# Performance work log

Hardware: AMD Instinct MI355X
Metric: run time of the kernel (lower is better)

## Reference

```python
import jax, jax.numpy as jnp
from jax import lax
import numpy as np
import math

# ---- static hyperparameters (from init_kwargs) ----
NUM_RAY = 64
NUM_RAY2 = NUM_RAY * NUM_RAY
NUM_SAMPLE = 64
STEP = 1.0 / (NUM_SAMPLE - 1)
RK = 3                       # RK4Range: neighbor cube side
K = 64                       # Num_RIGuassKernel per axis
PH = (192, 192, 192)         # PhantomSize (D, H, W)
THETA_X, THETA_Y, THETA_Z = 0.1, 0.05, 0.02
CENTER = (0.5, 0.5, 0.5)

# ---- constant neighbor offsets and kernel-center grids (Process_Parameter) ----
half = (RK - 1) // 2
_r = np.arange(-half, half + 1)
Xr_np, Yr_np, Zr_np = np.meshgrid(_r, _r, _r)
XR = jnp.asarray(Xr_np.flatten().reshape(1, RK ** 3), dtype=jnp.float32)
YR = jnp.asarray(Yr_np.flatten().reshape(1, RK ** 3), dtype=jnp.float32)
ZR = jnp.asarray(Zr_np.flatten().reshape(1, RK ** 3), dtype=jnp.float32)
_c = np.linspace(0, 1, K, dtype='float32')
Xc_np, Yc_np, Zc_np = np.meshgrid(_c, _c, _c)
XC = jnp.asarray(Xc_np.flatten())
YC = jnp.asarray(Yc_np.flatten())
ZC = jnp.asarray(Zc_np.flatten())

# ---- rotation matrices (Theta2TransMatrix) ----
def _build_transmats():
    def ry(t):
        c, s = math.cos(t), math.sin(t)
        return np.array([[1, 0, 0, 0], [0, c, -s, 0], [0, s, c, 0], [0, 0, 0, 1]], dtype=np.float64)
    def rx(t):
        c, s = math.cos(t), math.sin(t)
        return np.array([[c, 0, -s, 0], [0, 1, 0, 0], [s, 0, c, 0], [0, 0, 0, 1]], dtype=np.float64)
    def rz(t):
        c, s = math.cos(t), math.sin(t)
        return np.array([[c, -s, 0, 0], [s, c, 0, 0], [0, 0, 1, 0], [0, 0, 0, 1]], dtype=np.float64)
    RY, RY_ = ry(-THETA_Y), ry(THETA_Y)
    RX, RX_ = rx(THETA_X), rx(-THETA_X)
    RZ, RZ_ = rz(-THETA_Z), rz(THETA_Z)
    cx, cy, cz = CENTER
    S1 = np.eye(4); S1[3, :3] = [-cx, -cy, -cz]
    S2 = np.eye(4); S2[3, :3] = [cx, cy, cz]
    M_crd = S1 @ RZ @ RY @ RX @ S2
    M_drv = RX_ @ RY_ @ RZ_
    return jnp.asarray(M_crd, dtype=jnp.float32), jnp.asarray(M_drv, dtype=jnp.float32)

M_CRD, M_DRV = _build_transmats()


def _indexdist(x, y, z, RI):
    # x,y,z: [N]; RI: [K^3, 2] -> Gaussian-kernel interpolated n and spatial derivatives
    X, Y, Z = x[:, None], y[:, None], z[:, None]
    Xn = jnp.clip(jnp.round(X * K) + XR, 0.0, K - 1.0)
    Yn = jnp.clip(jnp.round(Y * K) + YR, 0.0, K - 1.0)
    Zn = jnp.clip(jnp.round(Z * K) + ZR, 0.0, K - 1.0)
    lin = (K * K * Yn + K * Xn + Zn).astype(jnp.int32)   # [N, RK^3]
    dx = XC[lin] - X
    dy = YC[lin] - Y
    dz = ZC[lin] - Z
    A = RI[lin, 0]
    sig = RI[lin, 1]
    inv_s2 = 1.0 / (sig * sig)
    ni = jnp.exp(-(dx * dx + dy * dy + dz * dz) * 0.5 * inv_s2) + 2e-7
    norm = jnp.sum(ni, axis=1)
    nu = ni * A
    nx = jnp.sum(nu * dx * inv_s2, axis=1)
    ny = jnp.sum(nu * dy * inv_s2, axis=1)
    nz = jnp.sum(nu * dz * inv_s2, axis=1)
    ndx = jnp.sum(ni * dx * inv_s2, axis=1)
    ndy = jnp.sum(ni * dy * inv_s2, axis=1)
    ndz = jnp.sum(ni * dz * inv_s2, axis=1)
    nu_s = jnp.sum(nu, axis=1)
    n = nu_s / norm
    inv_norm2 = 1.0 / (norm * norm)
    nx = (norm * nx - nu_s * ndx) * inv_norm2
    ny = (norm * ny - nu_s * ndy) * inv_norm2
    nz = (norm * nz - nu_s * ndz) * inv_norm2
    return n, nx, ny, nz


def _rayeq(z0, xy0, RI):
    ones = jnp.ones_like(z0)
    t = jnp.stack([xy0[:, 2], xy0[:, 0], z0, ones], axis=1) @ M_CRD
    n, dndx_, dndy_, dndz_ = _indexdist(t[:, 1], t[:, 0], t[:, 2], RI)
    d = jnp.stack([dndy_, dndx_, dndz_, ones], axis=1) @ M_DRV
    dndx, dndz, dndy = d[:, 1], d[:, 2], d[:, 0]
    dX1 = xy0[:, 1]
    dX2 = (dndx - dndz * dX1) * (1.0 + dX1 * dX1) / n
    dY1 = xy0[:, 3]
    dY2 = (dndy - dndz * dY1) * (1.0 + dY1 * dY1) / n
    return jnp.stack([dX1, dX2, dY1, dY2], axis=1)


def _ray_tracing(xyz0, RI):
    def step_fn(xyz, _):
        deriv = _rayeq(xyz[:, 4], xyz[:, 0:4], RI)
        xyzi = jnp.concatenate([xyz[:, 0:4] + deriv * STEP, (xyz[:, 4] + STEP)[:, None]], axis=1)
        return xyzi, xyzi
    _, rest = lax.scan(step_fn, xyz0, None, length=NUM_SAMPLE - 1)
    return jnp.concatenate([xyz0[None], rest], axis=0)   # [S, N, 5]


def _resize_axis_linear(a, axis, out_len):
    # align_corners=True 1D linear resize along `axis`
    in_len = a.shape[axis]
    pos = jnp.linspace(0.0, in_len - 1.0, out_len)
    i0 = jnp.clip(jnp.floor(pos).astype(jnp.int32), 0, in_len - 2)
    w = (pos - i0.astype(pos.dtype)).astype(a.dtype)
    a0 = jnp.take(a, i0, axis=axis)
    a1 = jnp.take(a, i0 + 1, axis=axis)
    shape = [1] * a.ndim
    shape[axis] = out_len
    w = w.reshape(shape)
    return a0 * (1.0 - w) + a1 * w


def _grid_sample_3d(vol, gx, gy, gz):
    # torch F.grid_sample trilinear, align_corners=True, padding_mode='zeros'
    D, H, W = vol.shape
    ix = (gx + 1.0) * 0.5 * (W - 1)
    iy = (gy + 1.0) * 0.5 * (H - 1)
    iz = (gz + 1.0) * 0.5 * (D - 1)
    x0 = jnp.floor(ix); y0 = jnp.floor(iy); z0 = jnp.floor(iz)
    fx = ix - x0; fy = iy - y0; fz = iz - z0
    out = jnp.zeros_like(ix)
    for dz in (0, 1):
        for dyy in (0, 1):
            for dxx in (0, 1):
                xi = x0 + dxx; yi = y0 + dyy; zi = z0 + dz
                wgt = (jnp.where(dxx == 1, fx, 1.0 - fx)
                       * jnp.where(dyy == 1, fy, 1.0 - fy)
                       * jnp.where(dz == 1, fz, 1.0 - fz))
                inb = ((xi >= 0) & (xi <= W - 1) & (yi >= 0) & (yi <= H - 1)
                       & (zi >= 0) & (zi <= D - 1))
                xc = jnp.clip(xi, 0, W - 1).astype(jnp.int32)
                yc = jnp.clip(yi, 0, H - 1).astype(jnp.int32)
                zc = jnp.clip(zi, 0, D - 1).astype(jnp.int32)
                out = out + jnp.where(inb, wgt * vol[zc, yc, xc], 0.0)
    return out


def setup_inputs() -> dict:
    key = jax.random.key(0)
    k1, k2, k3, k4, k5 = jax.random.split(key, 5)
    Phantom = jax.random.uniform(k1, (1, 1) + PH, dtype=jnp.float32)
    A = jax.random.uniform(k2, (K ** 3, 1), dtype=jnp.float32) * 0.9 + 0.1
    sig = jax.random.uniform(k3, (K ** 3, 1), dtype=jnp.float32) * 0.8 + 0.2
    RefractionIndex = jnp.concatenate([A, sig], axis=1)
    xy = jax.random.uniform(k4, (NUM_RAY2, 2), dtype=jnp.float32) * 0.8 + 0.1
    slopes = jax.random.normal(k5, (NUM_RAY2, 2), dtype=jnp.float32) * 0.05
    z0 = jnp.zeros((NUM_RAY2, 1), dtype=jnp.float32)
    # layout [x, dx/dz, y, dy/dz, z]
    RayInit = jnp.concatenate([xy[:, :1], slopes[:, :1], xy[:, 1:], slopes[:, 1:], z0], axis=1)
    return {"Phantom": Phantom, "RefractionIndex": RefractionIndex, "RayInit": RayInit}


def reference(Phantom, RefractionIndex, RayInit):
    RayInit = RayInit.reshape(NUM_RAY2, 5)
    RI = RefractionIndex.reshape(K ** 3, 2)
    paths = _ray_tracing(RayInit, RI)          # [S, N, 5]
    paths = paths * 2.0 - 1.0
    # paths -> [3, R, R, S] mesh of (x, y, z) coordinates
    mesh = jnp.stack([
        paths[:, :, 0].T.reshape(NUM_RAY, NUM_RAY, NUM_SAMPLE),
        paths[:, :, 2].T.reshape(NUM_RAY, NUM_RAY, NUM_SAMPLE),
        paths[:, :, 4].T.reshape(NUM_RAY, NUM_RAY, NUM_SAMPLE),
    ], axis=0)
    # trilinear resize (align_corners=True) to PhantomSize
    for ax, out_len in zip((1, 2, 3), PH):
        mesh = _resize_axis_linear(mesh, ax, out_len)   # [3, D, H, W]
    vol = Phantom.reshape(PH)
    out = _grid_sample_3d(vol, mesh[0], mesh[1], mesh[2])
    return out.reshape((1, 1) + PH)
```

## Files before the change

kernel.cpp:

```cpp
#include <hip/hip_runtime.h>
#include <math.h>

#define NRAY2 4096
#define NSAMP 64
#define PHD 192
#define PLANE (PHD*PHD)
constexpr float STEP = 1.0f / 63.0f;

struct Mats { float crd[16]; float drv[16]; };

static void mat_mul4(const double* A, const double* B, double* C) {
    for (int i = 0; i < 4; ++i)
        for (int j = 0; j < 4; ++j) {
            double s = 0.0;
            for (int k = 0; k < 4; ++k) s += A[i*4+k] * B[k*4+j];
            C[i*4+j] = s;
        }
}

static void build_mats(Mats& M) {
    const double tx = 0.1, ty = 0.05, tz = 0.02;
    const double cx = 0.5, cy = 0.5, cz = 0.5;
    auto ry = [](double t, double* m) {
        double c = cos(t), s = sin(t);
        double v[16] = {1,0,0,0, 0,c,-s,0, 0,s,c,0, 0,0,0,1};
        for (int i = 0; i < 16; ++i) m[i] = v[i];
    };
    auto rx = [](double t, double* m) {
        double c = cos(t), s = sin(t);
        double v[16] = {c,0,-s,0, 0,1,0,0, s,0,c,0, 0,0,0,1};
        for (int i = 0; i < 16; ++i) m[i] = v[i];
    };
    auto rz = [](double t, double* m) {
        double c = cos(t), s = sin(t);
        double v[16] = {c,-s,0,0, s,c,0,0, 0,0,1,0, 0,0,0,1};
        for (int i = 0; i < 16; ++i) m[i] = v[i];
    };
    double RY[16], RY_[16], RX[16], RX_[16], RZ[16], RZ_[16];
    ry(-ty, RY); ry(ty, RY_);
    rx(tx, RX);  rx(-tx, RX_);
    rz(-tz, RZ); rz(tz, RZ_);
    double S1[16] = {1,0,0,0, 0,1,0,0, 0,0,1,0, -cx,-cy,-cz,1};
    double S2[16] = {1,0,0,0, 0,1,0,0, 0,0,1,0,  cx, cy, cz,1};
    double t1[16], t2[16], t3[16], Mc[16], Md[16];
    mat_mul4(S1, RZ, t1);
    mat_mul4(t1, RY, t2);
    mat_mul4(t2, RX, t3);
    mat_mul4(t3, S2, Mc);
    mat_mul4(RX_, RY_, t1);
    mat_mul4(t1, RZ_, Md);
    for (int i = 0; i < 16; ++i) { M.crd[i] = (float)Mc[i]; M.drv[i] = (float)Md[i]; }
}

__device__ __forceinline__ float red32(float x) {
    int t;
    t = __builtin_amdgcn_update_dpp(0, __float_as_int(x), 0x121, 0xF, 0xF, true);
    x += __int_as_float(t);
    t = __builtin_amdgcn_update_dpp(0, __float_as_int(x), 0x122, 0xF, 0xF, true);
    x += __int_as_float(t);
    t = __builtin_amdgcn_update_dpp(0, __float_as_int(x), 0x124, 0xF, 0xF, true);
    x += __int_as_float(t);
    t = __builtin_amdgcn_update_dpp(0, __float_as_int(x), 0x128, 0xF, 0xF, true);
    x += __int_as_float(t);
    t = __builtin_amdgcn_ds_swizzle(__float_as_int(x), 0x401F);
    x += __int_as_float(t);
    return x;
}

__global__ __launch_bounds__(256) void ray_trace_kernel(
    const float* __restrict__ RI,
    const float* __restrict__ RayInit,
    float* __restrict__ meshXT,
    float* __restrict__ meshYT,
    Mats M)
{
    const int tid = threadIdx.x;
    const int nb  = tid & 31;
    const int ray = blockIdx.x * 8 + (tid >> 5);
    const bool act = nb < 27;

    float xr = 0.f, yr = 0.f, zr = 0.f;
    if (act) {
        int a0 = nb / 9, a1 = (nb / 3) % 3, a2 = nb % 3;
        xr = (float)(a1 - 1);
        yr = (float)(a0 - 1);
        zr = (float)(a2 - 1);
    }

    float X  = RayInit[ray*5 + 0];
    float dX = RayInit[ray*5 + 1];
    float Y  = RayInit[ray*5 + 2];
    float dY = RayInit[ray*5 + 3];
    float z  = RayInit[ray*5 + 4];

    if (nb == 0) meshXT[ray] = X*2.0f - 1.0f;
    if (nb == 1) meshYT[ray] = Y*2.0f - 1.0f;

    auto prep = [&](float pX, float pY, float pz,
                    float& ox, float& oy, float& oz,
                    float& oXn, float& oYn, float& oZn) -> const float2* {
        float x  = pY*M.crd[1] + pX*M.crd[5] + pz*M.crd[9]  + M.crd[13];
        float y  = pY*M.crd[0] + pX*M.crd[4] + pz*M.crd[8]  + M.crd[12];
        float zz = pY*M.crd[2] + pX*M.crd[6] + pz*M.crd[10] + M.crd[14];
        float XnL = __builtin_amdgcn_fmed3f(rintf(x *64.0f) + xr, 0.0f, 63.0f);
        float YnL = __builtin_amdgcn_fmed3f(rintf(y *64.0f) + yr, 0.0f, 63.0f);
        float ZnL = __builtin_amdgcn_fmed3f(rintf(zz*64.0f) + zr, 0.0f, 63.0f);
        int lin = (int)(YnL*4096.0f + XnL*64.0f + ZnL);
        ox = x; oy = y; oz = zz; oXn = XnL; oYn = YnL; oZn = ZnL;
        return (const float2*)RI + lin;
    };

    float cx_, cy_, cz_, Xn, Yn, Zn;
    float2 ri = *prep(X, Y, z, cx_, cy_, cz_, Xn, Yn, Zn);

    for (int s = 1; s < NSAMP; ++s) {
        float nX = X + dX*STEP, nY = Y + dY*STEP, nz = z + STEP;
        float ncx, ncy, ncz, nXn, nYn, nZn;
        float2 ri_n = *prep(nX, nY, nz, ncx, ncy, ncz, nXn, nYn, nZn);

        float dx = Xn*(1.0f/63.0f) - cx_;
        float dy = Yn*(1.0f/63.0f) - cy_;
        float dz = Zn*(1.0f/63.0f) - cz_;
        float inv_s2 = __builtin_amdgcn_rcpf(ri.y * ri.y);
        float e = __expf(-(dx*dx + dy*dy + dz*dz) * 0.5f * inv_s2) + 2e-7f;
        if (!act) e = 0.0f;
        float gdx = dx*inv_s2, gdy = dy*inv_s2, gdz = dz*inv_s2;
        float nu  = e * ri.x;

        float ni  = red32(e);
        float nuA = red32(nu);
        float sx  = red32(nu * gdx);
        float sy  = red32(nu * gdy);
        float sz  = red32(nu * gdz);
        float sdx = red32(e  * gdx);
        float sdy = red32(e  * gdy);
        float sdz = red32(e  * gdz);

        float r   = __builtin_amdgcn_rcpf(ni);
        float rn  = ni * __builtin_amdgcn_rcpf(nuA);
        float in2 = r * r;
        float gx_ = (ni*sx - nuA*sdx) * in2;
        float gy_ = (ni*sy - nuA*sdy) * in2;
        float gz_ = (ni*sz - nuA*sdz) * in2;

        float dndx = gy_*M.drv[1] + gx_*M.drv[5] + gz_*M.drv[9]  + M.drv[13];
        float dndy = gy_*M.drv[0] + gx_*M.drv[4] + gz_*M.drv[8]  + M.drv[12];
        float dndz = gy_*M.drv[2] + gx_*M.drv[6] + gz_*M.drv[10] + M.drv[14];

        float dX2 = (dndx - dndz*dX) * (1.0f + dX*dX) * rn;
        float dY2 = (dndy - dndz*dY) * (1.0f + dY*dY) * rn;

        X = nX; Y = nY; z = nz;
        dX += dX2 * STEP;
        dY += dY2 * STEP;

        if (nb == 0) meshXT[s*NRAY2 + ray] = X*2.0f - 1.0f;
        if (nb == 1) meshYT[s*NRAY2 + ray] = Y*2.0f - 1.0f;

        cx_ = ncx; cy_ = ncy; cz_ = ncz;
        Xn = nXn; Yn = nYn; Zn = nZn;
        ri = ri_n;
    }
}

typedef _Float16 h16;
typedef _Float16 h16v4 __attribute__((ext_vector_type(4)));

__global__ __launch_bounds__(1024) void sample_kernel(
    const float* __restrict__ vol,
    const float* __restrict__ meshXT,
    const float* __restrict__ meshYT,
    float* __restrict__ outDst,
    int transposed)
{
    __shared__ h16    plane_h[PLANE];
    __shared__ float2 slice[64*64];
    __shared__ float  wTab[PHD];
    __shared__ int    iTab[PHD];

    const int tid = threadIdx.x;
    const int blk = blockIdx.x;
    const int c = (blk >> 3) + 24 * (blk & 7);

    if (tid < PHD) {
        float p = tid * (63.0f / 191.0f);
        int i0 = min((int)p, 62);
        iTab[tid] = i0;
        wTab[tid] = p - (float)i0;
    }

    {
        const float4* src = (const float4*)(vol + c * PLANE);
        h16v4* dst = (h16v4*)plane_h;
        #pragma unroll
        for (int k = 0; k < (PLANE/4)/1024; ++k) {
            float4 v = src[tid + k*1024];
            h16v4 hv = {(h16)v.x, (h16)v.y, (h16)v.z, (h16)v.w};
            dst[tid + k*1024] = hv;
        }
    }

    float ps = c * (63.0f / 191.0f);
    int s0 = min((int)ps, 62);
    float wc = ps - (float)s0, wc0 = 1.0f - wc;
    {
        const float* x0 = meshXT + s0*NRAY2;
        const float* x1 = meshXT + (s0+1)*NRAY2;
        const float* y0 = meshYT + s0*NRAY2;
        const float* y1 = meshYT + (s0+1)*NRAY2;
        #pragma unroll
        for (int k = 0; k < 4096/1024; ++k) {
            int t = tid + k*1024;
            slice[t] = make_float2(x0[t]*wc0 + x1[t]*wc,
                                   y0[t]*wc0 + y1[t]*wc);
        }
    }
    __syncthreads();

    int a = tid / PHD, b = tid % PHD;
    #pragma unroll 2
    for (int k = 0; k < PLANE/1024; ++k) {
        int i0 = iTab[a]; float wa = wTab[a];
        int j0 = iTab[b]; float wb = wTab[b];

        float2 s00 = slice[i0*64 + j0];
        float2 s01 = slice[i0*64 + j0 + 1];
        float2 s10 = slice[(i0+1)*64 + j0];
        float2 s11 = slice[(i0+1)*64 + j0 + 1];

        float wb0 = 1.0f - wb, wa0 = 1.0f - wa;
        float gx = (s00.x*wb0 + s01.x*wb)*wa0 + (s10.x*wb0 + s11.x*wb)*wa;
        float gy = (s00.y*wb0 + s01.y*wb)*wa0 + (s10.y*wb0 + s11.y*wb)*wa;

        float ix = (gx + 1.0f) * 0.5f * 191.0f;
        float iy = (gy + 1.0f) * 0.5f * 191.0f;
        float x0f = floorf(ix); float fx = ix - x0f;
        float y0f = floorf(iy); float fy = iy - y0f;

        float acc = 0.0f;
        #pragma unroll
        for (int dyy = 0; dyy < 2; ++dyy) {
            #pragma unroll
            for (int dxx = 0; dxx < 2; ++dxx) {
                float xi = x0f + (float)dxx;
                float yi = y0f + (float)dyy;
                bool inb = (xi >= 0.0f) && (xi <= 191.0f) &&
                           (yi >= 0.0f) && (yi <= 191.0f);
                int xc = min(max((int)xi, 0), PHD - 1);
                int yc = min(max((int)yi, 0), PHD - 1);
                float w = (dxx ? fx : 1.0f - fx) * (dyy ? fy : 1.0f - fy);
                float val = (float)plane_h[yc*PHD + xc];
                acc += inb ? w * val : 0.0f;
            }
        }

        if (transposed) {
            outDst[c*PLANE + tid + k*1024] = acc;
        } else {
            outDst[(a*PHD + b)*PHD + c] = acc;
        }

        a += 5; b += 64;
        if (b >= PHD) { b -= PHD; a += 1; }
    }
}

__global__ __launch_bounds__(256) void transpose_kernel(
    const float* __restrict__ outT, float* __restrict__ out)
{
    __shared__ float t[32][33];
    const int a  = blockIdx.z;
    const int b0 = blockIdx.x * 32;
    const int c0 = blockIdx.y * 32;
    const int tx = threadIdx.x, ty = threadIdx.y;

    const float* src = outT + (size_t)(c0 + ty) * PLANE + a*PHD + b0 + tx;
    #pragma unroll
    for (int j = 0; j < 4; ++j)
        t[ty + 8*j][tx] = src[(size_t)(8*j) * PLANE];
    __syncthreads();

    float* dst = out + (size_t)a * PLANE + (size_t)(b0 + ty) * PHD + c0 + tx;
    #pragma unroll
    for (int j = 0; j < 4; ++j)
        dst[(size_t)(8*j) * PHD] = t[tx][ty + 8*j];
}

extern "C" void kernel_launch(void* const* d_in, const int* in_sizes, int n_in,
                              void* d_out, int out_size, void* d_ws, size_t ws_size,
                              hipStream_t stream)
{
    const float* Phantom = (const float*)d_in[0];
    const float* RI      = (const float*)d_in[1];
    const float* RayInit = (const float*)d_in[2];
    float* out = (float*)d_out;

    float* meshXT = (float*)d_ws;
    float* meshYT = meshXT + NRAY2 * NSAMP;
    float* outT   = meshYT + NRAY2 * NSAMP;

    const size_t need = (size_t)(2 * NRAY2 * NSAMP + PHD*PLANE) * sizeof(float);
    const int use_transpose = (ws_size >= need) ? 1 : 0;

    Mats M;
    build_mats(M);

    ray_trace_kernel<<<NRAY2/8, 256, 0, stream>>>(RI, RayInit, meshXT, meshYT, M);

    if (use_transpose) {
        sample_kernel<<<PHD, 1024, 0, stream>>>(Phantom, meshXT, meshYT, outT, 1);
        transpose_kernel<<<dim3(6, 6, PHD), dim3(32, 8), 0, stream>>>(outT, out);
    } else {
        sample_kernel<<<PHD, 1024, 0, stream>>>(Phantom, meshXT, meshYT, out, 0);
    }
}
```

Measured before the change: 156.3 us.

## Batch DPP reductions, store intermediate volume as fp16, widen transpose tiles

Ray tracing now interleaves its eight cross-lane reductions level by level, so independent DPP ops can overlap instead of running as serial chains. The intermediate transposed volume is written as half precision, which halves the traffic of writing and then re-reading it in the transpose pass. The transpose uses 64x64 tiles with fewer blocks. Rounding the sampled outputs to fp16 adds error of roughly 1e-3 relative, which could break the accuracy tolerance.

```diff
diff --git a/kernel.cpp b/kernel.cpp
--- a/kernel.cpp
+++ b/kernel.cpp
@@ -52,19 +52,27 @@
     for (int i = 0; i < 16; ++i) { M.crd[i] = (float)Mc[i]; M.drv[i] = (float)Md[i]; }
 }
 
-__device__ __forceinline__ float red32(float x) {
-    int t;
-    t = __builtin_amdgcn_update_dpp(0, __float_as_int(x), 0x121, 0xF, 0xF, true);
-    x += __int_as_float(t);
-    t = __builtin_amdgcn_update_dpp(0, __float_as_int(x), 0x122, 0xF, 0xF, true);
-    x += __int_as_float(t);
-    t = __builtin_amdgcn_update_dpp(0, __float_as_int(x), 0x124, 0xF, 0xF, true);
-    x += __int_as_float(t);
-    t = __builtin_amdgcn_update_dpp(0, __float_as_int(x), 0x128, 0xF, 0xF, true);
-    x += __int_as_float(t);
-    t = __builtin_amdgcn_ds_swizzle(__float_as_int(x), 0x401F);
-    x += __int_as_float(t);
-    return x;
+template<int CTRL>
+__device__ __forceinline__ void dpp_level8(float* v) {
+    int t[8];
+    #pragma unroll
+    for (int i = 0; i < 8; ++i)
+        t[i] = __builtin_amdgcn_update_dpp(0, __float_as_int(v[i]), CTRL, 0xF, 0xF, true);
+    #pragma unroll
+    for (int i = 0; i < 8; ++i) v[i] += __int_as_float(t[i]);
+}
+
+__device__ __forceinline__ void red8(float* v) {
+    dpp_level8<0x121>(v);
+    dpp_level8<0x122>(v);
+    dpp_level8<0x124>(v);
+    dpp_level8<0x128>(v);
+    int t[8];
+    #pragma unroll
+    for (int i = 0; i < 8; ++i)
+        t[i] = __builtin_amdgcn_ds_swizzle(__float_as_int(v[i]), 0x401F);
+    #pragma unroll
+    for (int i = 0; i < 8; ++i) v[i] += __int_as_float(t[i]);
 }
 
 __global__ __launch_bounds__(256) void ray_trace_kernel(
@@ -127,14 +135,11 @@
         float gdx = dx*inv_s2, gdy = dy*inv_s2, gdz = dz*inv_s2;
         float nu  = e * ri.x;
 
-        float ni  = red32(e);
-        float nuA = red32(nu);
-        float sx  = red32(nu * gdx);
-        float sy  = red32(nu * gdy);
-        float sz  = red32(nu * gdz);
-        float sdx = red32(e  * gdx);
-        float sdy = red32(e  * gdy);
-        float sdz = red32(e  * gdz);
+        float v[8] = { e, nu, nu*gdx, nu*gdy, nu*gdz, e*gdx, e*gdy, e*gdz };
+        red8(v);
+        float ni  = v[0], nuA = v[1];
+        float sx  = v[2], sy  = v[3], sz  = v[4];
+        float sdx = v[5], sdy = v[6], sdz = v[7];
 
         float r   = __builtin_amdgcn_rcpf(ni);
         float rn  = ni * __builtin_amdgcn_rcpf(nuA);
@@ -170,7 +175,8 @@
     const float* __restrict__ vol,
     const float* __restrict__ meshXT,
     const float* __restrict__ meshYT,
-    float* __restrict__ outDst,
+    h16*   __restrict__ outTh,
+    float* __restrict__ outDirect,
     int transposed)
 {
     __shared__ h16    plane_h[PLANE];
@@ -255,9 +261,9 @@
         }
 
         if (transposed) {
-            outDst[c*PLANE + tid + k*1024] = acc;
+            outTh[c*PLANE + tid + k*1024] = (h16)acc;
         } else {
-            outDst[(a*PHD + b)*PHD + c] = acc;
+            outDirect[(a*PHD + b)*PHD + c] = acc;
         }
 
         a += 5; b += 64;
@@ -266,24 +272,25 @@
 }
 
 __global__ __launch_bounds__(256) void transpose_kernel(
-    const float* __restrict__ outT, float* __restrict__ out)
+    const h16* __restrict__ outTh, float* __restrict__ out)
 {
-    __shared__ float t[32][33];
+    __shared__ h16 t[64][66];
     const int a  = blockIdx.z;
-    const int b0 = blockIdx.x * 32;
-    const int c0 = blockIdx.y * 32;
-    const int tx = threadIdx.x, ty = threadIdx.y;
-
-    const float* src = outT + (size_t)(c0 + ty) * PLANE + a*PHD + b0 + tx;
-    #pragma unroll
-    for (int j = 0; j < 4; ++j)
-        t[ty + 8*j][tx] = src[(size_t)(8*j) * PLANE];
+    const int b0 = blockIdx.x * 64;
+    const int c0 = blockIdx.y * 64;
+    const int tx = threadIdx.x & 63;
+    const int ty = threadIdx.x >> 6;
+
+    const h16* src = outTh + (size_t)(c0 + ty) * PLANE + a*PHD + b0 + tx;
+    #pragma unroll
+    for (int j = 0; j < 16; ++j)
+        t[ty + 4*j][tx] = src[(size_t)(4*j) * PLANE];
     __syncthreads();
 
     float* dst = out + (size_t)a * PLANE + (size_t)(b0 + ty) * PHD + c0 + tx;
     #pragma unroll
-    for (int j = 0; j < 4; ++j)
-        dst[(size_t)(8*j) * PHD] = t[tx][ty + 8*j];
+    for (int j = 0; j < 16; ++j)
+        dst[(size_t)(4*j) * PHD] = (float)t[tx][ty + 4*j];
 }
 
 extern "C" void kernel_launch(void* const* d_in, const int* in_sizes, int n_in,
@@ -297,9 +304,10 @@
 
     float* meshXT = (float*)d_ws;
     float* meshYT = meshXT + NRAY2 * NSAMP;
-    float* outT   = meshYT + NRAY2 * NSAMP;
-
-    const size_t need = (size_t)(2 * NRAY2 * NSAMP + PHD*PLANE) * sizeof(float);
+    h16*   outTh  = (h16*)(meshYT + NRAY2 * NSAMP);
+
+    const size_t need = (size_t)(2 * NRAY2 * NSAMP) * sizeof(float)
+                      + (size_t)PHD * PLANE * sizeof(h16);
     const int use_transpose = (ws_size >= need) ? 1 : 0;
 
     Mats M;
@@ -308,9 +316,11 @@
     ray_trace_kernel<<<NRAY2/8, 256, 0, stream>>>(RI, RayInit, meshXT, meshYT, M);
 
     if (use_transpose) {
-        sample_kernel<<<PHD, 1024, 0, stream>>>(Phantom, meshXT, meshYT, outT, 1);
-        transpose_kernel<<<dim3(6, 6, PHD), dim3(32, 8), 0, stream>>>(outT, out);
+        sample_kernel<<<PHD, 1024, 0, stream>>>(Phantom, meshXT, meshYT,
+                                                outTh, nullptr, 1);
+        transpose_kernel<<<dim3(3, 3, PHD), 256, 0, stream>>>(outTh, out);
     } else {
-        sample_kernel<<<PHD, 1024, 0, stream>>>(Phantom, meshXT, meshYT, out, 0);
-    }
-}
+        sample_kernel<<<PHD, 1024, 0, stream>>>(Phantom, meshXT, meshYT,
+                                                nullptr, out, 0);
+    }
+}
```

Result: no change. 157.8 us (+0.9%).
